# Kernel optimization log

Measured on AMD Instinct MI355X. Metric: run time of the kernel, lower is better.

Reference implementation:

```python
import jax, jax.numpy as jnp
import numpy as np

SEQ, D, H, P, FINAL = 2048, 1024, 16, 64, 1024


def setup_inputs() -> dict:
    key = jax.random.key(0)
    k_x, k_q, k_k, k_v, k_w = jax.random.split(key, 5)
    return {
        "x": jax.random.normal(k_x, (SEQ, D), dtype=jnp.float32),
        "Qw": jax.random.uniform(k_q, (H, D, P), dtype=jnp.float32),
        "Kw": jax.random.uniform(k_k, (H, D, P), dtype=jnp.float32),
        "Vw": jax.random.uniform(k_v, (H, D, P), dtype=jnp.float32),
        "W_fin": jax.random.normal(k_w, (H * P, FINAL), dtype=jnp.float32) * (1.0 / np.sqrt(H * P)),
        "b_fin": jnp.zeros((FINAL,), dtype=jnp.float32),
    }


def reference(x, Qw, Kw, Vw, W_fin, b_fin):
    # x: [S, D]; Qw/Kw/Vw: [H, D, P]
    Q = jnp.einsum("sd,hdp->hsp", x, Qw)  # [H, S, P]
    K = jnp.einsum("sd,hdp->hsp", x, Kw)
    V = jnp.einsum("sd,hdp->hsp", x, Vw)
    p_dim = K.shape[-1]
    # sigmoid attention: no row-wise normalization, scale by P (not sqrt(P))
    score = jax.nn.sigmoid(jnp.einsum("hsp,htp->hst", Q, K) / p_dim)  # [H, S, S]
    attn = jnp.einsum("hst,htp->hsp", score, V)  # [H, S, P]
    # faithful raw reshape (torch .reshape(seq, -1) on contiguous [H, S, P])
    concat = attn.reshape(x.shape[0], -1)  # [S, H*P]
    return concat @ W_fin + b_fin  # [S, FINAL]
```

## Files before the change

### kernel.cpp

```cpp
#include <hip/hip_runtime.h>
#include <hip/hip_bf16.h>

#define SEQL 2048
#define DMODEL 1024
#define NH 16
#define HEADP 64
#define FINALD 1024

using bf16x8 = __attribute__((ext_vector_type(8))) short;
using f32x4  = __attribute__((ext_vector_type(4))) float;
using f32x16 = __attribute__((ext_vector_type(16))) float;
using u32x4  = __attribute__((ext_vector_type(4))) unsigned;

#define WAITV(N) asm volatile("s_waitcnt vmcnt(" #N ")" ::: "memory")

__device__ __forceinline__ f32x4 mfma16(bf16x8 a, bf16x8 b, f32x4 c) {
  return __builtin_amdgcn_mfma_f32_16x16x32_bf16(a, b, c, 0, 0, 0);
}

__device__ __forceinline__ unsigned short f2bf(float f) {
  return __builtin_bit_cast(unsigned short, __float2bfloat16(f));
}

__device__ __forceinline__ void gload16(const void* g, void* l) {
  __builtin_amdgcn_global_load_lds(
      (const __attribute__((address_space(1))) void*)g,
      (__attribute__((address_space(3))) void*)l, 16, 0, 0);
}

__global__ __launch_bounds__(256) void k_prep(
    const float* __restrict__ Qw, const float* __restrict__ Kw,
    const float* __restrict__ Vw, const float* __restrict__ Wf,
    const float* __restrict__ x,
    unsigned short* __restrict__ Wt, unsigned short* __restrict__ WfT,
    unsigned short* __restrict__ xb) {
  __shared__ float tile[64][65];
  int z = blockIdx.z;
  int t = threadIdx.x;
  if (z == 4) {
    long i0 = ((long)blockIdx.y * 16 + blockIdx.x) * 2048 + t;
#pragma unroll
    for (int k = 0; k < 8; ++k) {
      long i = i0 + k * 256;
      float4 v = reinterpret_cast<const float4*>(x)[i];
      ushort4 o;
      o.x = f2bf(v.x); o.y = f2bf(v.y); o.z = f2bf(v.z); o.w = f2bf(v.w);
      reinterpret_cast<ushort4*>(xb)[i] = o;
    }
    return;
  }
  const float* src; unsigned short* dst;
  int C, tr = blockIdx.x * 64, tc;
  if (z < 3) {
    const float* s3 = (z == 0) ? Qw : (z == 1) ? Kw : Vw;
    src = s3 + (long)blockIdx.y * 65536;
    dst = Wt + (long)z * 1048576 + (long)blockIdx.y * 65536;
    C = 64; tc = 0;
  } else {
    src = Wf; dst = WfT; C = 1024; tc = blockIdx.y * 64;
  }
  const int R = 1024;
  int r0 = t >> 4, c4 = (t & 15) * 4;
#pragma unroll
  for (int i = 0; i < 4; ++i) {
    int r = i * 16 + r0;
    float4 v = *reinterpret_cast<const float4*>(src + (long)(tr + r) * C + tc + c4);
    tile[r][c4 + 0] = v.x; tile[r][c4 + 1] = v.y;
    tile[r][c4 + 2] = v.z; tile[r][c4 + 3] = v.w;
  }
  __syncthreads();
  int r4 = (t & 15) * 4, cc0 = t >> 4;
#pragma unroll
  for (int i = 0; i < 4; ++i) {
    int c = i * 16 + cc0;
    ushort4 o;
    o.x = f2bf(tile[r4 + 0][c]); o.y = f2bf(tile[r4 + 1][c]);
    o.z = f2bf(tile[r4 + 2][c]); o.w = f2bf(tile[r4 + 3][c]);
    *reinterpret_cast<ushort4*>(dst + (long)(tc + c) * R + tr + r4) = o;
  }
}

template <int EPI>
__global__ __launch_bounds__(256) void k_gemm(
    const unsigned short* __restrict__ A,
    const unsigned short* __restrict__ Bt,
    int K,
    unsigned short* __restrict__ Qb,
    unsigned short* __restrict__ Kb,
    unsigned short* __restrict__ Vtb,
    const float* __restrict__ bias,
    float* __restrict__ outf) {
  __shared__ char lds[49152];
  int flat = blockIdx.y * 16 + blockIdx.x;
  int cpx = (gridDim.x * gridDim.y) >> 3;
  flat = (flat & 7) * cpx + (flat >> 3);
  int m0 = (flat & 15) << 7, n0 = (flat >> 4) * 64;
  int t = threadIdx.x;
  int l = t & 63, w = t >> 6;
  int r = l & 15, g = l >> 4;
  int wr = w >> 1, wc = w & 1;

  const unsigned short* Arow = A + (long)m0 * K;
  const unsigned short* Brow = Bt + (long)n0 * K;
  int rr = l >> 2;
  int c8s = (((l & 3) ^ ((l >> 3) & 3)) * 8);

  auto stage = [&](int buf, int k0) {
    char* base = lds + buf * 24576;
#pragma unroll
    for (int kk = 0; kk < 2; ++kk) {
      char* dA = base + kk * 8192 + w * 2048;
      char* dB = base + 16384 + kk * 4096 + w * 1024;
      int kc = k0 + kk * 32 + c8s;
      gload16(Arow + (long)(w * 32 + rr) * K + kc, dA);
      gload16(Arow + (long)(w * 32 + 16 + rr) * K + kc, dA + 1024);
      gload16(Brow + (long)(w * 16 + rr) * K + kc, dB);
    }
  };

  int xk = (r >> 1) & 3;
  f32x4 acc[4][2] = {};
  int cur = 0, NK = K / 64;
  stage(0, 0);
  for (int kt = 0; kt < NK; ++kt) {
    __builtin_amdgcn_s_barrier();
    if (kt + 1 < NK) {
      stage(cur ^ 1, (kt + 1) * 64);
      WAITV(6);
    } else {
      WAITV(0);
    }
    __builtin_amdgcn_s_barrier();
    __builtin_amdgcn_sched_barrier(0);
    const char* base = lds + cur * 24576;
#pragma unroll
    for (int kk = 0; kk < 2; ++kk) {
      const char* As = base + kk * 8192;
      const char* Bs = base + 16384 + kk * 4096;
      bf16x8 af[4], bb[2];
#pragma unroll
      for (int i = 0; i < 4; ++i)
        af[i] = *reinterpret_cast<const bf16x8*>(As + (wr * 64 + i * 16 + r) * 64 + ((g ^ xk) * 16));
#pragma unroll
      for (int i = 0; i < 2; ++i)
        bb[i] = *reinterpret_cast<const bf16x8*>(Bs + (wc * 32 + i * 16 + r) * 64 + ((g ^ xk) * 16));
#pragma unroll
      for (int mi = 0; mi < 4; ++mi)
#pragma unroll
        for (int ni = 0; ni < 2; ++ni)
          acc[mi][ni] = mfma16(af[mi], bb[ni], acc[mi][ni]);
    }
    cur ^= 1;
  }

  if constexpr (EPI == 0) {
    int which = n0 >> 10;
    int hb = (n0 & 1023) >> 6;
    if (which < 2) {
      unsigned short* dst = (which == 0 ? Qb : Kb) + (long)hb * SEQL * HEADP;
#pragma unroll
      for (int mi = 0; mi < 4; ++mi) {
        int s0 = m0 + wr * 64 + mi * 16 + g * 4;
#pragma unroll
        for (int ni = 0; ni < 2; ++ni) {
          int p = wc * 32 + ni * 16 + r;
#pragma unroll
          for (int v = 0; v < 4; ++v)
            dst[(long)(s0 + v) * HEADP + p] = f2bf(acc[mi][ni][v]);
        }
      }
    } else {
      unsigned short* dst = Vtb + (long)hb * HEADP * SEQL;
#pragma unroll
      for (int mi = 0; mi < 4; ++mi) {
        int s0 = m0 + wr * 64 + mi * 16 + g * 4;
#pragma unroll
        for (int ni = 0; ni < 2; ++ni) {
          int p = wc * 32 + ni * 16 + r;
          ushort4 pk;
          pk.x = f2bf(acc[mi][ni][0]); pk.y = f2bf(acc[mi][ni][1]);
          pk.z = f2bf(acc[mi][ni][2]); pk.w = f2bf(acc[mi][ni][3]);
          *reinterpret_cast<ushort4*>(dst + (long)p * SEQL + s0) = pk;
        }
      }
    }
  } else {
#pragma unroll
    for (int ni = 0; ni < 2; ++ni) {
      int c = n0 + wc * 32 + ni * 16 + r;
      float bv = bias[c];
#pragma unroll
      for (int mi = 0; mi < 4; ++mi) {
        int s0 = m0 + wr * 64 + mi * 16 + g * 4;
#pragma unroll
        for (int v = 0; v < 4; ++v)
          outf[(long)(s0 + v) * FINALD + c] = acc[mi][ni][v] + bv;
      }
    }
  }
}

__global__ __launch_bounds__(512) void k_attn(
    const unsigned short* __restrict__ Qb,
    const unsigned short* __restrict__ Kb,
    const unsigned short* __restrict__ Vtb,
    unsigned short* __restrict__ Ab) {
  __shared__ char lds[65536];
  int b = blockIdx.x;
  int xcd = b & 7, j = b >> 3;
  int h = (xcd << 1) | (j & 1);
  int sblk = j >> 1;
  int q0b = sblk * 64;
  int tid = threadIdx.x;
  int lane = tid & 63, w = tid >> 6;
  int lo5 = lane & 31, hi = lane >> 5;
  int qg = w & 1, tpar = w >> 1;
  const unsigned short* Kh = Kb + (long)h * SEQL * HEADP;
  const unsigned short* Vh = Vtb + (long)h * HEADP * SEQL;
  const unsigned short* Qrow = Qb + ((long)h * SEQL + q0b + qg * 32 + lo5) * HEADP;

  bf16x8 qf[4];
#pragma unroll
  for (int ks = 0; ks < 4; ++ks)
    qf[ks] = *reinterpret_cast<const bf16x8*>(Qrow + ks * 16 + hi * 8);

  f32x16 zz = {};
  f32x16 oacc[2] = {zz, zz};
  const float CLN = -0.02254211001389005f;

  auto stage = [&](int buf, int t0) {
    char* kb = lds + buf * 32768 + w * 2048;
#pragma unroll
    for (int jj = 0; jj < 2; ++jj) {
      int row = w * 16 + jj * 8 + (lane >> 3);
      int c = (lane & 7) ^ (row & 7);
      gload16(Kh + (long)(t0 + row) * HEADP + c * 8, kb + jj * 1024);
    }
    char* vb = lds + buf * 32768 + 16384 + w * 2048;
#pragma unroll
    for (int jj = 0; jj < 2; ++jj) {
      int vr = w * 32 + jj * 16 + (lane >> 2);
      int p = vr & 63, tp = vr >> 6;
      int c = (lane & 3) ^ ((p >> 1) & 3);
      gload16(Vh + (long)p * SEQL + t0 + tp * 32 + c * 8, vb + jj * 1024);
    }
  };

  int cur = 0;
  stage(0, 0);
  for (int t0 = 0; t0 < SEQL; t0 += 128) {
    __builtin_amdgcn_s_barrier();
    if (t0 + 128 < SEQL) {
      stage(cur ^ 1, t0 + 128);
      WAITV(4);
    } else {
      WAITV(0);
    }
    __builtin_amdgcn_s_barrier();
    __builtin_amdgcn_sched_barrier(0);

    const char* kb = lds + cur * 32768;
    const char* vb = kb + 16384;
    int krow = tpar * 32 + lo5;

    f32x16 s = zz;
    __builtin_amdgcn_s_setprio(1);
#pragma unroll
    for (int ks = 0; ks < 4; ++ks) {
      int c = ks * 2 + hi;
      bf16x8 kf = *reinterpret_cast<const bf16x8*>(
          kb + krow * 128 + ((c ^ (krow & 7)) * 16));
      s = __builtin_amdgcn_mfma_f32_32x32x16_bf16(kf, qf[ks], s, 0, 0, 0);
    }
    __builtin_amdgcn_s_setprio(0);

    float p[16];
#pragma unroll
    for (int r = 0; r < 16; ++r) {
      float e = __builtin_amdgcn_exp2f(s[r] * CLN);
      p[r] = __builtin_amdgcn_rcpf(1.0f + e);
    }
    unsigned d[8];
#pragma unroll
    for (int gq = 0; gq < 2; ++gq) {
      unsigned x1, x2, y1, y2;
      asm("v_cvt_pk_bf16_f32 %0, %1, %2" : "=v"(x1) : "v"(p[gq*8+0]), "v"(p[gq*8+1]));
      asm("v_cvt_pk_bf16_f32 %0, %1, %2" : "=v"(x2) : "v"(p[gq*8+2]), "v"(p[gq*8+3]));
      asm("v_cvt_pk_bf16_f32 %0, %1, %2" : "=v"(y1) : "v"(p[gq*8+4]), "v"(p[gq*8+5]));
      asm("v_cvt_pk_bf16_f32 %0, %1, %2" : "=v"(y2) : "v"(p[gq*8+6]), "v"(p[gq*8+7]));
      asm volatile("v_permlane32_swap_b32 %0, %1" : "+v"(x1), "+v"(y1));
      asm volatile("v_permlane32_swap_b32 %0, %1" : "+v"(x2), "+v"(y2));
      d[gq*4+0] = x1; d[gq*4+1] = x2; d[gq*4+2] = y1; d[gq*4+3] = y2;
    }

    __builtin_amdgcn_s_setprio(1);
#pragma unroll
    for (int ts = 0; ts < 2; ++ts) {
      u32x4 pu = {d[ts*4+0], d[ts*4+1], d[ts*4+2], d[ts*4+3]};
      bf16x8 pa = __builtin_bit_cast(bf16x8, pu);
#pragma unroll
      for (int nb = 0; nb < 2; ++nb) {
        int prow = nb * 32 + lo5;
        int c = ts * 2 + hi;
        bf16x8 vf = *reinterpret_cast<const bf16x8*>(
            vb + tpar * 4096 + prow * 64 + ((c ^ ((prow >> 1) & 3)) * 16));
        oacc[nb] = __builtin_amdgcn_mfma_f32_32x32x16_bf16(pa, vf, oacc[nb], 0, 0, 0);
      }
    }
    __builtin_amdgcn_s_setprio(0);
    cur ^= 1;
  }

  __syncthreads();
  float* pr = (float*)(lds + tpar * 16384);
#pragma unroll
  for (int nb = 0; nb < 2; ++nb)
#pragma unroll
    for (int r = 0; r < 16; ++r) {
      int q = qg * 32 + (r & 3) + 8 * (r >> 2) + 4 * hi;
      pr[q * 64 + nb * 32 + lo5] = oacc[nb][r];
    }
  __syncthreads();
  int q = tid >> 3, pc = (tid & 7) * 8;
  unsigned short* Oh = Ab + ((long)h * SEQL + q0b + q) * HEADP + pc;
#pragma unroll
  for (int k = 0; k < 2; ++k) {
    float4 sum = *reinterpret_cast<const float4*>((const float*)lds + q * 64 + pc + k * 4);
#pragma unroll
    for (int par = 1; par < 4; ++par) {
      float4 v = *reinterpret_cast<const float4*>(
          (const float*)(lds + par * 16384) + q * 64 + pc + k * 4);
      sum.x += v.x; sum.y += v.y; sum.z += v.z; sum.w += v.w;
    }
    ushort4 o;
    o.x = f2bf(sum.x); o.y = f2bf(sum.y); o.z = f2bf(sum.z); o.w = f2bf(sum.w);
    *reinterpret_cast<ushort4*>(Oh + k * 4) = o;
  }
}

extern "C" void kernel_launch(void* const* d_in, const int* in_sizes, int n_in,
                              void* d_out, int out_size, void* d_ws, size_t ws_size,
                              hipStream_t stream) {
  const float* x  = (const float*)d_in[0];
  const float* Qw = (const float*)d_in[1];
  const float* Kw = (const float*)d_in[2];
  const float* Vw = (const float*)d_in[3];
  const float* Wf = (const float*)d_in[4];
  const float* bf = (const float*)d_in[5];
  float* out = (float*)d_out;

  unsigned short* ws  = (unsigned short*)d_ws;
  unsigned short* xb  = ws;
  unsigned short* Wt  = ws + 2097152;
  unsigned short* WfT = ws + 5242880;
  unsigned short* Qb  = ws + 6291456;
  unsigned short* Kb  = ws + 8388608;
  unsigned short* Vtb = ws + 10485760;
  unsigned short* Ab  = ws + 12582912;

  k_prep<<<dim3(16, 16, 5), 256, 0, stream>>>(Qw, Kw, Vw, Wf, x, Wt, WfT, xb);
  k_gemm<0><<<dim3(16, 48), 256, 0, stream>>>(xb, Wt, DMODEL, Qb, Kb, Vtb, nullptr, nullptr);
  k_attn<<<512, 512, 0, stream>>>(Qb, Kb, Vtb, Ab);
  k_gemm<1><<<dim3(16, 16), 256, 0, stream>>>(Ab, WfT, DMODEL, nullptr, nullptr, nullptr, bf, out);
}
```

Baseline: 72.11 us.

## Software-pipeline PV MFMA one tile behind and fold sigmoid scale into Q

The attention loop now loads V fragments at the start of each tile and runs the previous tile's P·V MFMAs right after the current QK^T MFMAs. This overlaps the sigmoid exp/rcp work with matrix-core work instead of serialising them, and a drain step after the loop handles the last tile. The sigmoid scale constant is folded into Q when the projection epilogue writes it, which removes a multiply per score element. Launch bounds now request 4 waves per SIMD, and the extra held fragments raise register pressure, which may cause spills under that occupancy target.

```diff
diff --git a/kernel.cpp b/kernel.cpp
--- a/kernel.cpp
+++ b/kernel.cpp
@@ -13,6 +13,8 @@
 using u32x4  = __attribute__((ext_vector_type(4))) unsigned;
 
 #define WAITV(N) asm volatile("s_waitcnt vmcnt(" #N ")" ::: "memory")
+
+#define QSCALE (-0.02254211001389005f)
 
 __device__ __forceinline__ f32x4 mfma16(bf16x8 a, bf16x8 b, f32x4 c) {
   return __builtin_amdgcn_mfma_f32_16x16x32_bf16(a, b, c, 0, 0, 0);
@@ -157,6 +159,7 @@
     int which = n0 >> 10;
     int hb = (n0 & 1023) >> 6;
     if (which < 2) {
+      float sc = (which == 0) ? QSCALE : 1.0f;
       unsigned short* dst = (which == 0 ? Qb : Kb) + (long)hb * SEQL * HEADP;
 #pragma unroll
       for (int mi = 0; mi < 4; ++mi) {
@@ -166,7 +169,7 @@
           int p = wc * 32 + ni * 16 + r;
 #pragma unroll
           for (int v = 0; v < 4; ++v)
-            dst[(long)(s0 + v) * HEADP + p] = f2bf(acc[mi][ni][v]);
+            dst[(long)(s0 + v) * HEADP + p] = f2bf(acc[mi][ni][v] * sc);
         }
       }
     } else {
@@ -200,7 +203,7 @@
   }
 }
 
-__global__ __launch_bounds__(512) void k_attn(
+__global__ __launch_bounds__(512, 4) void k_attn(
     const unsigned short* __restrict__ Qb,
     const unsigned short* __restrict__ Kb,
     const unsigned short* __restrict__ Vtb,
@@ -226,7 +229,6 @@
 
   f32x16 zz = {};
   f32x16 oacc[2] = {zz, zz};
-  const float CLN = -0.02254211001389005f;
 
   auto stage = [&](int buf, int t0) {
     char* kb = lds + buf * 32768 + w * 2048;
@@ -246,6 +248,8 @@
     }
   };
 
+  bf16x8 paPrev[2];
+  bf16x8 vfPrev[4];
   int cur = 0;
   stage(0, 0);
   for (int t0 = 0; t0 < SEQL; t0 += 128) {
@@ -263,6 +267,17 @@
     const char* vb = kb + 16384;
     int krow = tpar * 32 + lo5;
 
+    bf16x8 vfNew[4];
+#pragma unroll
+    for (int ts = 0; ts < 2; ++ts)
+#pragma unroll
+      for (int nb = 0; nb < 2; ++nb) {
+        int prow = nb * 32 + lo5;
+        int c = ts * 2 + hi;
+        vfNew[ts * 2 + nb] = *reinterpret_cast<const bf16x8*>(
+            vb + tpar * 4096 + prow * 64 + ((c ^ ((prow >> 1) & 3)) * 16));
+      }
+
     f32x16 s = zz;
     __builtin_amdgcn_s_setprio(1);
 #pragma unroll
@@ -272,12 +287,20 @@
           kb + krow * 128 + ((c ^ (krow & 7)) * 16));
       s = __builtin_amdgcn_mfma_f32_32x32x16_bf16(kf, qf[ks], s, 0, 0, 0);
     }
+    if (t0 > 0) {
+#pragma unroll
+      for (int ts = 0; ts < 2; ++ts)
+#pragma unroll
+        for (int nb = 0; nb < 2; ++nb)
+          oacc[nb] = __builtin_amdgcn_mfma_f32_32x32x16_bf16(
+              paPrev[ts], vfPrev[ts * 2 + nb], oacc[nb], 0, 0, 0);
+    }
     __builtin_amdgcn_s_setprio(0);
 
     float p[16];
 #pragma unroll
     for (int r = 0; r < 16; ++r) {
-      float e = __builtin_amdgcn_exp2f(s[r] * CLN);
+      float e = __builtin_amdgcn_exp2f(s[r]);
       p[r] = __builtin_amdgcn_rcpf(1.0f + e);
     }
     unsigned d[8];
@@ -292,24 +315,23 @@
       asm volatile("v_permlane32_swap_b32 %0, %1" : "+v"(x2), "+v"(y2));
       d[gq*4+0] = x1; d[gq*4+1] = x2; d[gq*4+2] = y1; d[gq*4+3] = y2;
     }
-
-    __builtin_amdgcn_s_setprio(1);
 #pragma unroll
     for (int ts = 0; ts < 2; ++ts) {
       u32x4 pu = {d[ts*4+0], d[ts*4+1], d[ts*4+2], d[ts*4+3]};
-      bf16x8 pa = __builtin_bit_cast(bf16x8, pu);
-#pragma unroll
-      for (int nb = 0; nb < 2; ++nb) {
-        int prow = nb * 32 + lo5;
-        int c = ts * 2 + hi;
-        bf16x8 vf = *reinterpret_cast<const bf16x8*>(
-            vb + tpar * 4096 + prow * 64 + ((c ^ ((prow >> 1) & 3)) * 16));
-        oacc[nb] = __builtin_amdgcn_mfma_f32_32x32x16_bf16(pa, vf, oacc[nb], 0, 0, 0);
-      }
-    }
-    __builtin_amdgcn_s_setprio(0);
+      paPrev[ts] = __builtin_bit_cast(bf16x8, pu);
+    }
+#pragma unroll
+    for (int i = 0; i < 4; ++i) vfPrev[i] = vfNew[i];
     cur ^= 1;
   }
+  __builtin_amdgcn_s_setprio(1);
+#pragma unroll
+  for (int ts = 0; ts < 2; ++ts)
+#pragma unroll
+    for (int nb = 0; nb < 2; ++nb)
+      oacc[nb] = __builtin_amdgcn_mfma_f32_32x32x16_bf16(
+          paPrev[ts], vfPrev[ts * 2 + nb], oacc[nb], 0, 0, 0);
+  __builtin_amdgcn_s_setprio(0);
 
   __syncthreads();
   float* pr = (float*)(lds + tpar * 16384);
```

Measured after the change: 72.15 us. No clear change (+0.0%).

## Move W_fin transpose into attention launch and fold sigmoid scale into Q

Applied to the files above, without the earlier changes.

The W_fin transpose/bf16 conversion moves out of the prep kernel and into 256 extra blocks appended to the attention grid, so it can fill idle CUs alongside attention instead of lengthening the prep kernel. The sigmoid's -log2(e)/P scale is applied once in the QKV GEMM epilogue when writing Q, which removes a per-element multiply in the attention inner loop. Scaling Q before rounding to bf16 changes rounding slightly. The extra blocks add scheduling tail risk to the attention kernel.

```diff
diff --git a/kernel.cpp b/kernel.cpp
--- a/kernel.cpp
+++ b/kernel.cpp
@@ -14,6 +14,8 @@
 
 #define WAITV(N) asm volatile("s_waitcnt vmcnt(" #N ")" ::: "memory")
 
+#define QSCALE (-0.02254211001389005f)
+
 __device__ __forceinline__ f32x4 mfma16(bf16x8 a, bf16x8 b, f32x4 c) {
   return __builtin_amdgcn_mfma_f32_16x16x32_bf16(a, b, c, 0, 0, 0);
 }
@@ -30,14 +32,12 @@
 
 __global__ __launch_bounds__(256) void k_prep(
     const float* __restrict__ Qw, const float* __restrict__ Kw,
-    const float* __restrict__ Vw, const float* __restrict__ Wf,
-    const float* __restrict__ x,
-    unsigned short* __restrict__ Wt, unsigned short* __restrict__ WfT,
-    unsigned short* __restrict__ xb) {
+    const float* __restrict__ Vw, const float* __restrict__ x,
+    unsigned short* __restrict__ Wt, unsigned short* __restrict__ xb) {
   __shared__ float tile[64][65];
   int z = blockIdx.z;
   int t = threadIdx.x;
-  if (z == 4) {
+  if (z == 3) {
     long i0 = ((long)blockIdx.y * 16 + blockIdx.x) * 2048 + t;
 #pragma unroll
     for (int k = 0; k < 8; ++k) {
@@ -49,22 +49,16 @@
     }
     return;
   }
-  const float* src; unsigned short* dst;
-  int C, tr = blockIdx.x * 64, tc;
-  if (z < 3) {
-    const float* s3 = (z == 0) ? Qw : (z == 1) ? Kw : Vw;
-    src = s3 + (long)blockIdx.y * 65536;
-    dst = Wt + (long)z * 1048576 + (long)blockIdx.y * 65536;
-    C = 64; tc = 0;
-  } else {
-    src = Wf; dst = WfT; C = 1024; tc = blockIdx.y * 64;
-  }
-  const int R = 1024;
+  const float* s3 = (z == 0) ? Qw : (z == 1) ? Kw : Vw;
+  const float* src = s3 + (long)blockIdx.y * 65536;
+  unsigned short* dst = Wt + (long)z * 1048576 + (long)blockIdx.y * 65536;
+  const int C = 64, R = 1024;
+  int tr = blockIdx.x * 64;
   int r0 = t >> 4, c4 = (t & 15) * 4;
 #pragma unroll
   for (int i = 0; i < 4; ++i) {
     int r = i * 16 + r0;
-    float4 v = *reinterpret_cast<const float4*>(src + (long)(tr + r) * C + tc + c4);
+    float4 v = *reinterpret_cast<const float4*>(src + (long)(tr + r) * C + c4);
     tile[r][c4 + 0] = v.x; tile[r][c4 + 1] = v.y;
     tile[r][c4 + 2] = v.z; tile[r][c4 + 3] = v.w;
   }
@@ -76,7 +70,7 @@
     ushort4 o;
     o.x = f2bf(tile[r4 + 0][c]); o.y = f2bf(tile[r4 + 1][c]);
     o.z = f2bf(tile[r4 + 2][c]); o.w = f2bf(tile[r4 + 3][c]);
-    *reinterpret_cast<ushort4*>(dst + (long)(tc + c) * R + tr + r4) = o;
+    *reinterpret_cast<ushort4*>(dst + (long)c * R + tr + r4) = o;
   }
 }
 
@@ -157,6 +151,7 @@
     int which = n0 >> 10;
     int hb = (n0 & 1023) >> 6;
     if (which < 2) {
+      float sc = (which == 0) ? QSCALE : 1.0f;
       unsigned short* dst = (which == 0 ? Qb : Kb) + (long)hb * SEQL * HEADP;
 #pragma unroll
       for (int mi = 0; mi < 4; ++mi) {
@@ -166,7 +161,7 @@
           int p = wc * 32 + ni * 16 + r;
 #pragma unroll
           for (int v = 0; v < 4; ++v)
-            dst[(long)(s0 + v) * HEADP + p] = f2bf(acc[mi][ni][v]);
+            dst[(long)(s0 + v) * HEADP + p] = f2bf(acc[mi][ni][v] * sc);
         }
       }
     } else {
@@ -204,14 +199,47 @@
     const unsigned short* __restrict__ Qb,
     const unsigned short* __restrict__ Kb,
     const unsigned short* __restrict__ Vtb,
-    unsigned short* __restrict__ Ab) {
+    unsigned short* __restrict__ Ab,
+    const float* __restrict__ Wf,
+    unsigned short* __restrict__ WfT) {
   __shared__ char lds[65536];
   int b = blockIdx.x;
+  int tid = threadIdx.x;
+
+  if (b >= 512) {
+    int u = b - 512;
+    int tr = (u & 15) * 64, tc = (u >> 4) * 64;
+    float (*tile)[65] = (float(*)[65])lds;
+    int t = tid;
+    if (t < 256) {
+      int r0 = t >> 4, c4 = (t & 15) * 4;
+#pragma unroll
+      for (int i = 0; i < 4; ++i) {
+        int r = i * 16 + r0;
+        float4 v = *reinterpret_cast<const float4*>(Wf + (long)(tr + r) * 1024 + tc + c4);
+        tile[r][c4 + 0] = v.x; tile[r][c4 + 1] = v.y;
+        tile[r][c4 + 2] = v.z; tile[r][c4 + 3] = v.w;
+      }
+    }
+    __syncthreads();
+    if (t < 256) {
+      int r4 = (t & 15) * 4, cc0 = t >> 4;
+#pragma unroll
+      for (int i = 0; i < 4; ++i) {
+        int c = i * 16 + cc0;
+        ushort4 o;
+        o.x = f2bf(tile[r4 + 0][c]); o.y = f2bf(tile[r4 + 1][c]);
+        o.z = f2bf(tile[r4 + 2][c]); o.w = f2bf(tile[r4 + 3][c]);
+        *reinterpret_cast<ushort4*>(WfT + (long)(tc + c) * 1024 + tr + r4) = o;
+      }
+    }
+    return;
+  }
+
   int xcd = b & 7, j = b >> 3;
   int h = (xcd << 1) | (j & 1);
   int sblk = j >> 1;
   int q0b = sblk * 64;
-  int tid = threadIdx.x;
   int lane = tid & 63, w = tid >> 6;
   int lo5 = lane & 31, hi = lane >> 5;
   int qg = w & 1, tpar = w >> 1;
@@ -226,7 +254,6 @@
 
   f32x16 zz = {};
   f32x16 oacc[2] = {zz, zz};
-  const float CLN = -0.02254211001389005f;
 
   auto stage = [&](int buf, int t0) {
     char* kb = lds + buf * 32768 + w * 2048;
@@ -277,7 +304,7 @@
     float p[16];
 #pragma unroll
     for (int r = 0; r < 16; ++r) {
-      float e = __builtin_amdgcn_exp2f(s[r] * CLN);
+      float e = __builtin_amdgcn_exp2f(s[r]);
       p[r] = __builtin_amdgcn_rcpf(1.0f + e);
     }
     unsigned d[8];
@@ -358,8 +385,8 @@
   unsigned short* Vtb = ws + 10485760;
   unsigned short* Ab  = ws + 12582912;
 
-  k_prep<<<dim3(16, 16, 5), 256, 0, stream>>>(Qw, Kw, Vw, Wf, x, Wt, WfT, xb);
+  k_prep<<<dim3(16, 16, 4), 256, 0, stream>>>(Qw, Kw, Vw, x, Wt, xb);
   k_gemm<0><<<dim3(16, 48), 256, 0, stream>>>(xb, Wt, DMODEL, Qb, Kb, Vtb, nullptr, nullptr);
-  k_attn<<<512, 512, 0, stream>>>(Qb, Kb, Vtb, Ab);
+  k_attn<<<768, 512, 0, stream>>>(Qb, Kb, Vtb, Ab, Wf, WfT);
   k_gemm<1><<<dim3(16, 16), 256, 0, stream>>>(Ab, WfT, DMODEL, nullptr, nullptr, nullptr, bf, out);
 }
```

Result: no change. 71.25 us (-1.2%).
